# Optimization experiments

Hardware: AMD Instinct MI355X
Metric: run time of the kernel (lower is better)

The kernel has to match this reference:

```python
import jax, jax.numpy as jnp
import numpy as np

B, F, HU, HC = 8192, 100, 128, 512


def _lin(key, din, dout, bias=True, scale=0.02):
    k1, k2 = jax.random.split(key)
    w = jax.random.normal(k1, (din, dout), jnp.float32) * scale
    if bias:
        b = jax.random.normal(k2, (dout,), jnp.float32) * scale
        return w, b
    return (w,)


def setup_inputs() -> dict:
    key = jax.random.key(0)
    ks = jax.random.split(key, 24)
    d = {}
    d['feature_list'] = jax.random.normal(ks[0], (B, F), jnp.float32)
    d['is_treat'] = jax.random.uniform(ks[1], (B,), jnp.float32)
    d['emb'] = jax.random.normal(ks[2], (F, HU), jnp.float32) * 0.02
    d['t_w'], d['t_b'] = _lin(ks[3], 1, HU)
    d['qw'], d['qb'] = _lin(ks[4], HU, HU)
    d['kw'], d['kb'] = _lin(ks[5], HU, HU)
    d['vw'], d['vb'] = _lin(ks[6], HU, HU)
    (d['a1w'],) = _lin(ks[7], HU, HU, bias=False)
    d['a2w'], d['a2b'] = _lin(ks[8], HU, HU)
    (d['a3w'],) = _lin(ks[9], HU, 1, bias=False)
    d['c1w'], d['c1b'] = _lin(ks[10], F * HU, HC)
    d['c2w'], d['c2b'] = _lin(ks[11], HC, HC)
    d['c3w'], d['c3b'] = _lin(ks[12], HC, HC // 2)
    d['c4w'], d['c4b'] = _lin(ks[13], HC // 2, HC // 4)
    d['c5w'], d['c5b'] = _lin(ks[14], HC // 4, HC // 8)
    d['clw'], d['clb'] = _lin(ks[15], HC // 8, 1)
    d['ctw'], d['ctb'] = _lin(ks[16], HC // 8, 1)
    d['u1w'], d['u1b'] = _lin(ks[17], HU, HU)
    d['u2w'], d['u2b'] = _lin(ks[18], HU, HU // 2)
    d['u3w'], d['u3b'] = _lin(ks[19], HU // 2, HU // 4)
    d['u4w'], d['u4b'] = _lin(ks[20], HU // 4, HU // 8)
    d['tlw'], d['tlb'] = _lin(ks[21], HU // 8, 1)
    d['utw'], d['utb'] = _lin(ks[22], HU // 8, 1)
    return d


def reference(feature_list, is_treat, emb, t_w, t_b, qw, qb, kw, kb, vw, vb,
              a1w, a2w, a2b, a3w, c1w, c1b, c2w, c2b, c3w, c3b, c4w, c4b,
              c5w, c5b, clw, clb, ctw, ctb, u1w, u1b, u2w, u2b, u3w, u3b,
              u4w, u4b, tlw, tlb, utw, utb):
    elu = jax.nn.elu
    sig = jax.nn.sigmoid
    b, f = feature_list.shape
    h = emb.shape[1]
    # per-feature embedding: [B, F, H]
    x_rep = feature_list[:, :, None] * emb[None, :, :]
    # normalize over the feature axis (dim=1), as in torch.linalg.norm(dim=1)
    nx = x_rep / jnp.linalg.norm(x_rep, axis=1, keepdims=True)
    # self-attention with sigmoid-then-softmax scores
    Q = nx @ qw + qb
    K = nx @ kw + kb
    V = nx @ vw + vb
    scores = jnp.einsum('bfh,bgh->bfg', Q, K) / (h ** 0.5)
    attn_w = jax.nn.softmax(sig(scores), axis=-1)
    xx = jnp.einsum('bfg,bgh->bfh', attn_w, V).reshape(b, f * h)
    # control net tower
    c = elu(xx @ c1w + c1b)
    c = elu(c @ c2w + c2b)
    c = elu(c @ c3w + c3b)
    c = elu(c @ c4w + c4b)
    c = elu(c @ c5w + c5b)  # is_self=True
    c_logit = c @ clw + clb
    c_tau = c @ ctw + ctb
    c_prob = sig(c_logit)
    # treatment representation: Linear(1, hu) on ones -> [B, H]
    t_rep = jnp.ones((b, 1), feature_list.dtype) @ t_w.reshape(1, h) + t_b
    # interaction attention (vectorized over features)
    att = jax.nn.relu(sig(t_rep @ a1w)[:, None, :] + sig(x_rep @ a2w + a2b))
    att = (att @ a3w)[..., 0]  # [B, F]
    attn = jax.nn.softmax(att, axis=1)
    xt = jnp.einsum('bf,bfh->bh', attn, x_rep)
    # uplift net tower
    u = elu(xt @ u1w + u1b)
    u = elu(u @ u2w + u2b)
    u = elu(u @ u3w + u3b)
    u = elu(u @ u4w + u4b)  # is_self=True
    t_logit = u @ tlw + tlb
    u_tau = u @ utw + utb
    t_prob = sig(t_logit)
    return (c_logit, c_prob, c_tau, t_logit, t_prob, u_tau)
```

## Files before the change

### kernel.cpp

```cpp
#include <hip/hip_runtime.h>
#include <hip/hip_bf16.h>

typedef __bf16 bf16;
typedef __bf16 bf16x8 __attribute__((ext_vector_type(8)));
typedef __bf16 bf16x4 __attribute__((ext_vector_type(4)));
typedef float f32x4 __attribute__((ext_vector_type(4)));
typedef unsigned u32x4 __attribute__((ext_vector_type(4)));

#define DEVI static __device__ __forceinline__

DEVI float sigmoidf_(float x){ return 1.0f/(1.0f+__expf(-x)); }
DEVI float eluf_(float x){ return x>0.f ? x : (__expf(x)-1.f); }
DEVI f32x4 mfma16(bf16x8 a, bf16x8 b, f32x4 c){ return __builtin_amdgcn_mfma_f32_16x16x32_bf16(a,b,c,0,0,0); }
DEVI f32x4 mfma8(long a, long b, f32x4 c){ return __builtin_amdgcn_mfma_f32_16x16x32_fp8_fp8(a,b,c,0,0,0); }
DEVI unsigned pack2_(float a, float b){
    union { bf16 v[2]; unsigned u; } t; t.v[0]=(bf16)a; t.v[1]=(bf16)b; return t.u;
}
DEVI unsigned long long pack4_(float a, float b, float c, float d){
    union { bf16 v[4]; unsigned long long u; } t;
    t.v[0]=(bf16)a; t.v[1]=(bf16)b; t.v[2]=(bf16)c; t.v[3]=(bf16)d; return t.u;
}
DEVI unsigned cvtfp8x4_(float a, float b, float c, float d){
    int v = __builtin_amdgcn_cvt_pk_fp8_f32(a, b, 0, false);
    v = __builtin_amdgcn_cvt_pk_fp8_f32(c, d, v, true);
    return (unsigned)v;
}

#define B_ 8192
#define F_ 100
#define FP 112
#define H_ 128
#define KC_ 12800
#define SPLIT_ 2
#define FP8SC 16.0f

#define SWZ(r,bc) ((bc) ^ (((r)&7)<<4))

DEVI void dotrans_(float (*t)[33], const float* in, bf16* out, int R, int C, int bx, int by, int tid){
    int c0 = bx*32, r0 = by*32;
    int tc = tid & 31, tr = tid >> 5;
    #pragma unroll
    for (int i=0;i<4;i++){
        int r = tr + i*8;
        t[r][tc] = in[(size_t)(r0+r)*C + c0 + tc];
    }
    __syncthreads();
    #pragma unroll
    for (int i=0;i<4;i++){
        int ro = tr + i*8;
        out[(size_t)(c0+ro)*R + r0 + tc] = (bf16)t[tc][ro];
    }
}

__global__ void k_prep_all(const float* __restrict__ qw, const float* __restrict__ qb,
                           const float* __restrict__ kw, const float* __restrict__ kb,
                           const float* __restrict__ tw, const float* __restrict__ tb,
                           const float* __restrict__ a1w, const float* __restrict__ vw,
                           const float* __restrict__ a2w, const float* __restrict__ c2w,
                           const float* __restrict__ c3w,
                           bf16* __restrict__ mextT, float* __restrict__ sigt, float* __restrict__ cconst,
                           bf16* __restrict__ wvT, bf16* __restrict__ wa2t,
                           bf16* __restrict__ c2wt, bf16* __restrict__ c3wt){
    __shared__ float t[32][33];
    const float rsc = 0.08838834764831845f;
    int blk = blockIdx.x, tid = threadIdx.x;
    if (blk < 9){
        #pragma unroll 1
        for (int e=0; e<8; ++e){
            int idx = e*256 + tid;
            int n = blk*16 + (idx>>7), h = idx&127;
            float acc = 0.f;
            if (n < 128){
                for (int d=0; d<128; ++d) acc += qw[h*128+d]*kw[n*128+d];
            } else if (n == 128){
                for (int d=0; d<128; ++d) acc += qw[h*128+d]*kb[d];
            } else if (n == 129){
                for (int d=0; d<128; ++d) acc += kw[h*128+d]*qb[d];
            }
            mextT[n*128+h] = (bf16)(acc*rsc);
        }
    } else if (blk == 9){
        if (tid < 128){
            float acc = 0.f;
            for (int h=0; h<128; ++h) acc += (tw[h]+tb[h]) * a1w[h*128+tid];
            sigt[tid] = sigmoidf_(acc);
        } else if (tid == 128){
            float acc = 0.f;
            for (int d=0; d<128; ++d) acc += qb[d]*kb[d];
            cconst[0] = acc*rsc;
        }
    } else if (blk < 26){
        int i = blk-10; dotrans_(t, vw, wvT, 128,128, i&3, i>>2, tid);
    } else if (blk < 42){
        int i = blk-26; dotrans_(t, a2w, wa2t, 128,128, i&3, i>>2, tid);
    } else if (blk < 298){
        int i = blk-42; dotrans_(t, c2w, c2wt, 512,512, i&15, i>>4, tid);
    } else {
        int i = blk-298; dotrans_(t, c3w, c3wt, 512,256, i&7, i>>3, tid);
    }
}

DEVI int kappa_(int k){
    int f = k>>7, h = k&127;
    if (f < 96)
        return (((f>>4)<<3) | (h>>4))*256 + ((f&15)>>2)*64 + (h&15)*4 + (f&3);
    else
        return 12288 + (h>>4)*64 + (h&15)*4 + (f&3);
}
__global__ void k_tc_kappa8(const float* __restrict__ in, unsigned char* __restrict__ out){
    __shared__ float t[32][33];
    const int C = 512;
    int c0 = blockIdx.x*32, r0 = blockIdx.y*32;
    int tc = threadIdx.x & 31, tr = threadIdx.x >> 5;
    #pragma unroll
    for (int i=0;i<4;i++){
        int r = tr + i*8;
        t[r][tc] = in[(size_t)(r0+r)*C + c0 + tc];
    }
    __syncthreads();
    #pragma unroll
    for (int i=0;i<4;i++){
        int ro = tr + i*8;
        float x = t[tc][ro]*FP8SC;
        int v = __builtin_amdgcn_cvt_pk_fp8_f32(x, x, 0, false);
        out[(size_t)(c0+ro)*KC_ + kappa_(r0+tc)] = (unsigned char)v;
    }
}

__global__ __launch_bounds__(256,2) void k_gatt(
    const float* __restrict__ feat, const float* __restrict__ emb,
    const bf16* __restrict__ wa2t, const float* __restrict__ a2b,
    const float* __restrict__ a3w, const float* __restrict__ sigt,
    float* __restrict__ attg)
{
    __shared__ bf16 sAt[128][136];
    __shared__ bf16 sBt[128][136];
    __shared__ float sRed[2][128];
    int tid=threadIdx.x, w=tid>>6, lane=tid&63, l15=lane&15, l4=lane>>4;
    int m0 = blockIdx.x*128;
    int wr = w>>1, wc = w&1;
    f32x4 acc[4][4];
    #pragma unroll
    for(int mi=0;mi<4;mi++)
        #pragma unroll
        for(int ni=0;ni<4;ni++) acc[mi][ni] = (f32x4){0.f,0.f,0.f,0.f};

    #pragma unroll 2
    for (int t8=0; t8<8; t8++){
        int v = tid + t8*256;
        int row = v>>4, colg = (v&15)*8;
        int gr = m0+row;
        int bb = gr/112, ff = gr - bb*112;
        bf16x8 o;
        if (ff < F_){
            float fv = feat[(size_t)bb*F_ + ff];
            const float* ep = emb + ff*H_ + colg;
            f32x4 e0 = *(const f32x4*)ep;
            f32x4 e1 = *(const f32x4*)(ep+4);
            o[0]=(bf16)(fv*e0[0]); o[1]=(bf16)(fv*e0[1]); o[2]=(bf16)(fv*e0[2]); o[3]=(bf16)(fv*e0[3]);
            o[4]=(bf16)(fv*e1[0]); o[5]=(bf16)(fv*e1[1]); o[6]=(bf16)(fv*e1[2]); o[7]=(bf16)(fv*e1[3]);
        } else {
            #pragma unroll
            for (int e=0;e<8;e++) o[e]=(bf16)0.f;
        }
        *(bf16x8*)&sAt[row][colg] = o;
        *(bf16x8*)&sBt[row][colg] = *(const bf16x8*)(wa2t + row*H_ + colg);
    }
    __syncthreads();
    #pragma unroll
    for(int ks=0;ks<4;ks++){
        bf16x8 af[4], bfr[4];
        #pragma unroll
        for(int mi=0;mi<4;mi++) af[mi] = *(const bf16x8*)&sAt[wr*64+mi*16+l15][ks*32+l4*8];
        #pragma unroll
        for(int ni=0;ni<4;ni++) bfr[ni] = *(const bf16x8*)&sBt[wc*64+ni*16+l15][ks*32+l4*8];
        #pragma unroll
        for(int mi=0;mi<4;mi++)
            #pragma unroll
            for(int ni=0;ni<4;ni++)
                acc[mi][ni] = mfma16(af[mi], bfr[ni], acc[mi][ni]);
    }
    float sg[4], ab[4], a3[4];
    #pragma unroll
    for (int ni=0;ni<4;ni++){
        int n = wc*64 + ni*16 + l15;
        sg[ni]=sigt[n]; ab[ni]=a2b[n]; a3[ni]=a3w[n];
    }
    #pragma unroll
    for (int mi=0;mi<4;mi++){
        float sj[4] = {0.f,0.f,0.f,0.f};
        #pragma unroll
        for (int ni=0;ni<4;ni++){
            #pragma unroll
            for (int j=0;j<4;j++){
                float u = sigmoidf_(acc[mi][ni][j] + ab[ni]);
                float t = sg[ni] + u;
                t = t>0.f ? t : 0.f;
                sj[j] += t*a3[ni];
            }
        }
        #pragma unroll
        for (int j=0;j<4;j++){
            float v = sj[j];
            #pragma unroll
            for (int m=1;m<16;m<<=1) v += __shfl_xor(v,m,16);
            sj[j]=v;
        }
        if (l15==0){
            #pragma unroll
            for (int j=0;j<4;j++) sRed[wc][wr*64+mi*16+l4*4+j] = sj[j];
        }
    }
    __syncthreads();
    if (tid < 128) attg[(size_t)m0 + tid] = sRed[0][tid] + sRed[1][tid];
}

__global__ __launch_bounds__(512,2) void k_attn2(
    const float* __restrict__ feat, const float* __restrict__ emb,
    const bf16* __restrict__ mextT, const bf16* __restrict__ wvT,
    const float* __restrict__ vb, const float* __restrict__ cconst,
    const float* __restrict__ attg,
    unsigned char* __restrict__ xxb, bf16* __restrict__ xtb)
{
    __shared__ char L[81792];
    char* Lm = L;
    char* Ln = L + 32768;
    float* sFeat  = (float*)(L+61440);
    float* sAw    = (float*)(L+61888);
    float* normP  = (float*)(L+62336);
    float* xtP    = (float*)(L+66432);
    float* sNorm  = (float*)(L+79872);
    float* sAlpha = (float*)(L+80384);
    float* sBeta  = (float*)(L+80832);
    float* sInv   = (float*)(L+81280);

    int b = blockIdx.x;
    int tid = threadIdx.x, w = tid>>6, lane = tid&63;
    int l15 = lane&15, l4 = lane>>4;
    bf16 (*sP)[72] = (bf16(*)[72])(L + 61440 + w*2304);

    bf16x8 awv[4];
    #pragma unroll
    for (int kc=0;kc<4;kc++)
        awv[kc] = *(const bf16x8*)(wvT + (w*16+l15)*H_ + kc*32 + l4*8);
    float vbr = vb[w*16+l15];

    #pragma unroll 2
    for (int v = tid; v < 128*16; v += 512){
        int n = v >> 4, cg = (v & 15) * 8;
        *(u32x4*)(Lm + n*256 + SWZ(n, cg*2)) = *(const u32x4*)(mextT + n*128 + cg);
    }
    if (tid < FP) sFeat[tid] = (tid<F_) ? feat[(size_t)b*F_+tid] : 0.f;
    if (w==0){
        const float* ag = attg + (size_t)b*FP;
        float a0 = (lane<F_)? ag[lane] : -1e30f;
        float a1 = (lane+64<F_)? ag[lane+64] : -1e30f;
        float m = fmaxf(a0,a1);
        #pragma unroll
        for(int s=1;s<64;s<<=1) m = fmaxf(m, __shfl_xor(m,s,64));
        float e0 = (lane<F_)? __expf(a0-m):0.f;
        float e1 = (lane+64<F_)? __expf(a1-m):0.f;
        float s = e0+e1;
        #pragma unroll
        for(int t=1;t<64;t<<=1) s += __shfl_xor(s,t,64);
        float inv = 1.f/s;
        if (lane<FP) sAw[lane] = e0*inv;
        if (lane+64<FP) sAw[lane+64] = e1*inv;
    }
    __syncthreads();

    int hp = (tid&63)*2, gg = tid>>6;
    {
        float fa0=0.f, fa1=0.f;
        #pragma unroll 4
        for (int it=0; it<13; ++it){
            int f = gg + 8*it;
            if (f < F_){
                float2 e2 = *(const float2*)(emb + f*H_ + hp);
                float v0 = sFeat[f]*e2.x, v1 = sFeat[f]*e2.y;
                fa0 += v0*v0; fa1 += v1*v1;
            }
        }
        *(float2*)(normP + gg*128 + hp) = make_float2(fa0, fa1);
    }
    __syncthreads();
    if (tid < 128){
        float s = 0.f;
        #pragma unroll
        for (int g2=0; g2<8; ++g2) s += normP[g2*128 + tid];
        sNorm[tid] = sqrtf(s);
    }
    __syncthreads();

    {
        float rn0 = __builtin_amdgcn_rcpf(sNorm[hp]);
        float rn1 = __builtin_amdgcn_rcpf(sNorm[hp+1]);
        #pragma unroll 4
        for (int it=0; it<13; ++it){
            int f = gg + 8*it;
            if (f < F_){
                float2 e2 = *(const float2*)(emb + f*H_ + hp);
                *(unsigned*)(Ln + f*256 + SWZ(f, hp*2)) = pack2_(sFeat[f]*e2.x*rn0, sFeat[f]*e2.y*rn1);
            }
        }
        for (int z=tid; z<768; z+=512){
            int f = 100 + (z>>6), hz = (z&63)*2;
            *(unsigned*)(Ln + f*256 + SWZ(f, hz*2)) = 0u;
        }
    }
    __syncthreads();

    int mt = w;

    if (mt < 7){
        bf16x8 bfr8[4];
        #pragma unroll
        for (int kc=0;kc<4;kc++)
            bfr8[kc] = *(const bf16x8*)(mextT + (128+(l15&1))*H_ + kc*32 + l4*8);
        f32x4 acc = {0.f,0.f,0.f,0.f};
        #pragma unroll
        for (int kc=0;kc<4;kc++){
            bf16x8 a = *(const bf16x8*)(Ln + (mt*16+l15)*256 + SWZ(mt*16+l15, (kc*32+l4*8)*2));
            acc = mfma16(a, bfr8[kc], acc);
        }
        if (l15==0){
            #pragma unroll
            for (int j=0;j<4;j++) sAlpha[mt*16+l4*4+j] = acc[j];
        }
        if (l15==1){
            #pragma unroll
            for (int j=0;j<4;j++) sBeta[mt*16+l4*4+j] = acc[j];
        }
    }
    {
        int g4 = tid>>7, h = tid&127;
        float acc=0.f;
        #pragma unroll 5
        for (int it=0; it<25; ++it){
            int f = g4 + 4*it;
            acc += sAw[f] * (float)*(const bf16*)(Ln + f*256 + SWZ(f, h*2));
        }
        xtP[g4*128+h] = acc;
    }
    __syncthreads();
    if (tid < 128)
        xtb[(size_t)b*H_+tid] = (bf16)((xtP[tid]+xtP[128+tid]+xtP[256+tid]+xtP[384+tid]) * sNorm[tid]);
    __syncthreads();

    const float cc = cconst[0];
    unsigned long long uexB[3];
    if (mt < 7){
        bf16x8 afxi[4];
        #pragma unroll
        for (int kc=0;kc<4;kc++)
            afxi[kc] = *(const bf16x8*)(Ln + (mt*16+l15)*256 + SWZ(mt*16+l15, (kc*32+l4*8)*2));
        f32x4 sc[7];
        #pragma unroll
        for (int gt=0; gt<7; gt++) sc[gt] = (f32x4){0.f,0.f,0.f,0.f};
        #pragma unroll 1
        for (int p=0; p<2; p++){
            #pragma unroll 2
            for (int nt4=0; nt4<4; nt4++){
                int nt = p*4 + nt4;
                bf16x8 bw[4];
                #pragma unroll
                for (int kc=0;kc<4;kc++)
                    bw[kc] = *(const bf16x8*)(Lm + (nt*16+l15)*256 + SWZ(nt*16+l15, (kc*32+l4*8)*2));
                f32x4 d = {0.f,0.f,0.f,0.f};
                #pragma unroll
                for (int kc=0;kc<4;kc++) d = mfma16(bw[kc], afxi[kc], d);
                *(unsigned long long*)(&sP[l15][nt4*16 + l4*4]) = pack4_(d[0],d[1],d[2],d[3]);
            }
            bf16x8 afs0 = *(const bf16x8*)&sP[l15][l4*8];
            bf16x8 afs1 = *(const bf16x8*)&sP[l15][32+l4*8];
            #pragma unroll
            for (int gt=0; gt<7; gt++){
                int r = gt*16+l15;
                bf16x8 b0 = *(const bf16x8*)(Ln + r*256 + SWZ(r, (p*64 + l4*8)*2));
                bf16x8 b1 = *(const bf16x8*)(Ln + r*256 + SWZ(r, (p*64 + 32 + l4*8)*2));
                sc[gt] = mfma16(b0, afs0, sc[gt]);
                sc[gt] = mfma16(b1, afs1, sc[gt]);
            }
        }
        float aj = sAlpha[mt*16+l15];
        float rs = 0.f;
        #pragma unroll
        for (int gt=0; gt<7; gt++){
            f32x4 bt4 = *(const f32x4*)&sBeta[gt*16+l4*4];
            float e[4];
            #pragma unroll
            for (int j=0;j<4;j++){
                int g = gt*16 + l4*4 + j;
                float val = sc[gt][j] + aj + bt4[j] + cc;
                e[j] = (g<F_) ? __expf(sigmoidf_(val)) : 0.f;
                rs += e[j];
            }
            if (gt < 4)
                *(unsigned long long*)(&sP[l15][gt*16 + l4*4]) = pack4_(e[0],e[1],e[2],e[3]);
            else
                uexB[gt-4] = pack4_(e[0],e[1],e[2],e[3]);
        }
        rs += __shfl_xor(rs, 16, 64);
        rs += __shfl_xor(rs, 32, 64);
        if (l4 == 0) sInv[w*16 + l15] = 1.f/rs;
    }

    unsigned long long vpku[7];
    #pragma unroll
    for (int gt=0; gt<7; gt++){
        f32x4 acc = {0.f,0.f,0.f,0.f};
        #pragma unroll
        for (int kc=0;kc<4;kc++){
            int r = gt*16+l15;
            bf16x8 a = *(const bf16x8*)(Ln + r*256 + SWZ(r, (kc*32+l4*8)*2));
            acc = mfma16(a, awv[kc], acc);
        }
        vpku[gt] = pack4_(acc[0]+vbr, acc[1]+vbr, acc[2]+vbr, acc[3]+vbr);
    }
    __syncthreads();

    {
        int hrow = w*16 + l15;
        #pragma unroll
        for (int gt=0; gt<7; gt++)
            *(unsigned long long*)(Lm + hrow*256 + SWZ(hrow, gt*32 + l4*8)) = vpku[gt];
    }
    __syncthreads();

    if (mt < 7){
        bf16x8 ap0 = *(const bf16x8*)&sP[l15][l4*8];
        bf16x8 ap1 = *(const bf16x8*)&sP[l15][32+l4*8];
        f32x4 acc8[8];
        #pragma unroll
        for (int ht=0;ht<8;ht++) acc8[ht] = (f32x4){0.f,0.f,0.f,0.f};
        #pragma unroll
        for (int ht=0; ht<8; ht++){
            int r = ht*16+l15;
            bf16x8 bv0 = *(const bf16x8*)(Lm + r*256 + SWZ(r, (l4*8)*2));
            bf16x8 bv1 = *(const bf16x8*)(Lm + r*256 + SWZ(r, (32+l4*8)*2));
            acc8[ht] = mfma16(ap0, bv0, acc8[ht]);
            acc8[ht] = mfma16(ap1, bv1, acc8[ht]);
        }
        #pragma unroll
        for (int gt=4; gt<7; gt++)
            *(unsigned long long*)(&sP[l15][(gt-4)*16 + l4*4]) = uexB[gt-4];
        *(unsigned long long*)(&sP[l15][48 + l4*4]) = 0ull;
        bf16x8 ap2 = *(const bf16x8*)&sP[l15][l4*8];
        bf16x8 ap3 = *(const bf16x8*)&sP[l15][32+l4*8];
        #pragma unroll
        for (int ht=0; ht<8; ht++){
            int r = ht*16+l15;
            int c2 = 64+l4*8;
            int c3 = 96+l4*8;  if (c3 >= 112) c3 = 96;
            bf16x8 bv2 = *(const bf16x8*)(Lm + r*256 + SWZ(r, c2*2));
            bf16x8 bv3 = *(const bf16x8*)(Lm + r*256 + SWZ(r, c3*2));
            acc8[ht] = mfma16(ap2, bv2, acc8[ht]);
            acc8[ht] = mfma16(ap3, bv3, acc8[ht]);
        }
        float fs[4];
        #pragma unroll
        for (int j=0;j<4;j++) fs[j] = sInv[w*16 + l4*4 + j] * FP8SC;
        #pragma unroll
        for (int ht=0; ht<8; ht++){
            unsigned u = cvtfp8x4_(acc8[ht][0]*fs[0], acc8[ht][1]*fs[1], acc8[ht][2]*fs[2], acc8[ht][3]*fs[3]);
            if (mt < 6){
                *(unsigned*)(xxb + (size_t)b*KC_ + (mt*8+ht)*256 + lane*4) = u;
            } else if (l4 == 0){
                *(unsigned*)(xxb + (size_t)b*KC_ + 12288 + ht*64 + l15*4) = u;
            }
        }
    }
}

__global__ __launch_bounds__(256,2) void k_gemm_fp8(const unsigned char* __restrict__ A,
        const unsigned char* __restrict__ Bt, float* __restrict__ part, int M, int N, int K, int KS)
{
    __shared__ unsigned char sA[128][72];
    __shared__ unsigned char sB[128][72];
    int tid=threadIdx.x, w=tid>>6, lane=tid&63, l15=lane&15, l4=lane>>4;
    int m0 = blockIdx.y*128, n0 = blockIdx.x*128;
    int kbeg = blockIdx.z*KS, kend = kbeg + KS;
    int wr = w>>1, wc = w&1;
    f32x4 acc[4][4];
    #pragma unroll
    for(int mi=0;mi<4;mi++)
        #pragma unroll
        for(int ni=0;ni<4;ni++) acc[mi][ni] = (f32x4){0.f,0.f,0.f,0.f};

    for (int k0=kbeg; k0<kend; k0+=64){
        __syncthreads();
        #pragma unroll
        for (int t2=0;t2<2;t2++){
            int t = tid + t2*256;
            int row=t>>2, col=(t&3)*16;
            *(u32x4*)&sA[row][col] = *(const u32x4*)(A + (size_t)(m0+row)*K + k0 + col);
            *(u32x4*)&sB[row][col] = *(const u32x4*)(Bt + (size_t)(n0+row)*K + k0 + col);
        }
        __syncthreads();
        #pragma unroll
        for(int ks=0;ks<2;ks++){
            long af[4], bfr[4];
            #pragma unroll
            for(int mi=0;mi<4;mi++) af[mi] = *(const long*)&sA[wr*64+mi*16+l15][ks*32+l4*8];
            #pragma unroll
            for(int ni=0;ni<4;ni++) bfr[ni] = *(const long*)&sB[wc*64+ni*16+l15][ks*32+l4*8];
            #pragma unroll
            for(int mi=0;mi<4;mi++)
                #pragma unroll
                for(int ni=0;ni<4;ni++)
                    acc[mi][ni] = mfma8(af[mi], bfr[ni], acc[mi][ni]);
        }
    }
    float* pz = part + (size_t)blockIdx.z*M*N;
    #pragma unroll
    for(int mi=0;mi<4;mi++)
        #pragma unroll
        for(int ni=0;ni<4;ni++){
            int col = n0 + wc*64 + ni*16 + l15;
            #pragma unroll
            for(int j=0;j<4;j++){
                int row = m0 + wr*64 + mi*16 + l4*4 + j;
                pz[(size_t)row*N + col] = acc[mi][ni][j];
            }
        }
}

__global__ void k_c1fin(const float* __restrict__ part, const float* __restrict__ bias,
                        bf16* __restrict__ out){
    const size_t MN = (size_t)B_*512;
    size_t e0 = ((size_t)blockIdx.x*256 + threadIdx.x)*4;
    f32x4 s = *(const f32x4*)(part + e0);
    s += *(const f32x4*)(part + MN + e0);
    f32x4 bb = *(const f32x4*)(bias + (e0 & 511));
    const float ds = 1.0f/(FP8SC*FP8SC);
    unsigned long long u = pack4_(eluf_(s[0]*ds+bb[0]), eluf_(s[1]*ds+bb[1]),
                                  eluf_(s[2]*ds+bb[2]), eluf_(s[3]*ds+bb[3]));
    *(unsigned long long*)(out + e0) = u;
}

template<int BN, bool ELU>
__global__ __launch_bounds__(256,2) void k_gemm(const bf16* __restrict__ A, const bf16* __restrict__ Bt,
        const float* __restrict__ bias, bf16* __restrict__ out, int M, int N, int K)
{
    __shared__ bf16 sAt[128][72];
    __shared__ bf16 sBt[BN][72];
    int tid=threadIdx.x, w=tid>>6, lane=tid&63, l15=lane&15, l4=lane>>4;
    int m0 = blockIdx.y*128, n0 = blockIdx.x*BN;
    constexpr int MI = (BN==128)?4:2;
    constexpr int NI = (BN==128)?4:BN/16;
    int wr = (BN==128)? (w>>1) : w;
    int wc = (BN==128)? (w&1) : 0;
    f32x4 acc[MI][NI];
    #pragma unroll
    for(int mi=0;mi<MI;mi++)
        #pragma unroll
        for(int ni=0;ni<NI;ni++) acc[mi][ni] = (f32x4){0.f,0.f,0.f,0.f};

    for (int k0=0; k0<K; k0+=64){
        __syncthreads();
        for (int t=tid; t<128*8; t+=256){
            int row=t>>3, col=(t&7)*8;
            *(bf16x8*)&sAt[row][col] = *(const bf16x8*)(A + (size_t)(m0+row)*K + k0 + col);
        }
        for (int t=tid; t<BN*8; t+=256){
            int row=t>>3, col=(t&7)*8;
            *(bf16x8*)&sBt[row][col] = *(const bf16x8*)(Bt + (size_t)(n0+row)*K + k0 + col);
        }
        __syncthreads();
        #pragma unroll
        for(int ks=0;ks<2;ks++){
            bf16x8 af[MI], bfr[NI];
            #pragma unroll
            for(int mi=0;mi<MI;mi++) af[mi] = *(const bf16x8*)&sAt[wr*(MI*16)+mi*16+l15][ks*32+l4*8];
            #pragma unroll
            for(int ni=0;ni<NI;ni++) bfr[ni] = *(const bf16x8*)&sBt[wc*64+ni*16+l15][ks*32+l4*8];
            #pragma unroll
            for(int mi=0;mi<MI;mi++)
                #pragma unroll
                for(int ni=0;ni<NI;ni++)
                    acc[mi][ni] = mfma16(af[mi], bfr[ni], acc[mi][ni]);
        }
    }
    #pragma unroll
    for(int mi=0;mi<MI;mi++)
        #pragma unroll
        for(int ni=0;ni<NI;ni++){
            int col = n0 + wc*64 + ni*16 + l15;
            float bc = bias[col];
            #pragma unroll
            for(int j=0;j<4;j++){
                int row = m0 + wr*(MI*16) + mi*16 + l4*4 + j;
                float v = acc[mi][ni][j] + bc;
                if (ELU) v = eluf_(v);
                out[(size_t)row*N + col] = (bf16)v;
            }
        }
}

__global__ __launch_bounds__(256,2) void k_ctail(const bf16* __restrict__ c3o,
    const float* __restrict__ c4w, const float* __restrict__ c4b,
    const float* __restrict__ c5w, const float* __restrict__ c5b,
    const float* __restrict__ clw, const float* __restrict__ clb,
    const float* __restrict__ ctw, const float* __restrict__ ctb, float* __restrict__ outp)
{
    __shared__ float sA[32][260];
    __shared__ float sB[32][132];
    __shared__ float sC[32][68];
    int tid = threadIdx.x; int r0 = blockIdx.x*32;
    for (int v=tid; v<32*64; v+=256){
        int r=v>>6, c=(v&63)*4;
        bf16x4 x = *(const bf16x4*)(c3o + (size_t)(r0+r)*256 + c);
        sA[r][c]=(float)x[0]; sA[r][c+1]=(float)x[1]; sA[r][c+2]=(float)x[2]; sA[r][c+3]=(float)x[3];
    }
    __syncthreads();
    {
        int j = tid&127, rb = tid>>7;
        float acc[16];
        #pragma unroll
        for (int i=0;i<16;i++) acc[i]=c4b[j];
        #pragma unroll 4
        for (int h=0;h<256;h++){
            float wv = c4w[h*128+j];
            #pragma unroll
            for (int i=0;i<16;i++) acc[i] += sA[2*i+rb][h]*wv;
        }
        #pragma unroll
        for (int i=0;i<16;i++) sB[2*i+rb][j] = eluf_(acc[i]);
    }
    __syncthreads();
    {
        int j = tid&63, rb = tid>>6;
        float acc[8];
        #pragma unroll
        for (int i=0;i<8;i++) acc[i]=c5b[j];
        #pragma unroll 4
        for (int h=0;h<128;h++){
            float wv = c5w[h*64+j];
            #pragma unroll
            for (int i=0;i<8;i++) acc[i] += sB[4*i+rb][h]*wv;
        }
        #pragma unroll
        for (int i=0;i<8;i++) sC[4*i+rb][j] = eluf_(acc[i]);
    }
    __syncthreads();
    if (tid < 32){
        float r1 = clb[0], r2 = ctb[0];
        #pragma unroll 8
        for (int k=0;k<64;k++){ float v = sC[tid][k]; r1 += v*clw[k]; r2 += v*ctw[k]; }
        int row = r0 + tid;
        outp[row] = r1;
        outp[B_ + row] = sigmoidf_(r1);
        outp[(size_t)2*B_ + row] = r2;
    }
}

__global__ __launch_bounds__(256,2) void k_utower(const bf16* __restrict__ xtb,
    const float* __restrict__ u1w, const float* __restrict__ u1b,
    const float* __restrict__ u2w, const float* __restrict__ u2b,
    const float* __restrict__ u3w, const float* __restrict__ u3b,
    const float* __restrict__ u4w, const float* __restrict__ u4b,
    const float* __restrict__ tlw, const float* __restrict__ tlb,
    const float* __restrict__ utw, const float* __restrict__ utb, float* __restrict__ outp)
{
    __shared__ float sA[32][132];
    __shared__ float sB[32][132];
    __shared__ float sC[32][68];
    __shared__ float sD[32][36];
    __shared__ float sE[32][20];
    int tid = threadIdx.x; int r0 = blockIdx.x*32;
    for (int v=tid; v<32*32; v+=256){
        int r=v>>5, c=(v&31)*4;
        bf16x4 x = *(const bf16x4*)(xtb + (size_t)(r0+r)*128 + c);
        sA[r][c]=(float)x[0]; sA[r][c+1]=(float)x[1]; sA[r][c+2]=(float)x[2]; sA[r][c+3]=(float)x[3];
    }
    __syncthreads();
    {
        int j = tid&127, rb = tid>>7;
        float acc[16];
        #pragma unroll
        for (int i=0;i<16;i++) acc[i]=u1b[j];
        #pragma unroll 4
        for (int h=0;h<128;h++){
            float wv = u1w[h*128+j];
            #pragma unroll
            for (int i=0;i<16;i++) acc[i] += sA[2*i+rb][h]*wv;
        }
        #pragma unroll
        for (int i=0;i<16;i++) sB[2*i+rb][j] = eluf_(acc[i]);
    }
    __syncthreads();
    {
        int j = tid&63, rb = tid>>6;
        float acc[8];
        #pragma unroll
        for (int i=0;i<8;i++) acc[i]=u2b[j];
        #pragma unroll 4
        for (int h=0;h<128;h++){
            float wv = u2w[h*64+j];
            #pragma unroll
            for (int i=0;i<8;i++) acc[i] += sB[4*i+rb][h]*wv;
        }
        #pragma unroll
        for (int i=0;i<8;i++) sC[4*i+rb][j] = eluf_(acc[i]);
    }
    __syncthreads();
    {
        int j = tid&31, rb = tid>>5;
        float acc[4];
        #pragma unroll
        for (int i=0;i<4;i++) acc[i]=u3b[j];
        #pragma unroll 4
        for (int h=0;h<64;h++){
            float wv = u3w[h*32+j];
            #pragma unroll
            for (int i=0;i<4;i++) acc[i] += sC[8*i+rb][h]*wv;
        }
        #pragma unroll
        for (int i=0;i<4;i++) sD[8*i+rb][j] = eluf_(acc[i]);
    }
    __syncthreads();
    {
        int j = tid&15, rb = tid>>4;
        float acc0=u4b[j], acc1=u4b[j];
        #pragma unroll 4
        for (int h=0;h<32;h++){
            float wv = u4w[h*16+j];
            acc0 += sD[rb][h]*wv;
            acc1 += sD[16+rb][h]*wv;
        }
        sE[rb][j] = eluf_(acc0);
        sE[16+rb][j] = eluf_(acc1);
    }
    __syncthreads();
    if (tid < 32){
        float r1 = tlb[0], r2 = utb[0];
        #pragma unroll
        for (int k=0;k<16;k++){ float v = sE[tid][k]; r1 += v*tlw[k]; r2 += v*utw[k]; }
        int row = r0 + tid;
        outp[(size_t)3*B_ + row] = r1;
        outp[(size_t)4*B_ + row] = sigmoidf_(r1);
        outp[(size_t)5*B_ + row] = r2;
    }
}

extern "C" void kernel_launch(void* const* d_in, const int* in_sizes, int n_in,
                              void* d_out, int out_size, void* d_ws, size_t ws_size,
                              hipStream_t stream) {
    const float* feat=(const float*)d_in[0];
    const float* emb =(const float*)d_in[2];
    const float* t_w =(const float*)d_in[3]; const float* t_b=(const float*)d_in[4];
    const float* qw  =(const float*)d_in[5]; const float* qb =(const float*)d_in[6];
    const float* kw  =(const float*)d_in[7]; const float* kb =(const float*)d_in[8];
    const float* vw  =(const float*)d_in[9]; const float* vb =(const float*)d_in[10];
    const float* a1w =(const float*)d_in[11];
    const float* a2w =(const float*)d_in[12]; const float* a2b=(const float*)d_in[13];
    const float* a3w =(const float*)d_in[14];
    const float* c1w =(const float*)d_in[15]; const float* c1b=(const float*)d_in[16];
    const float* c2w =(const float*)d_in[17]; const float* c2b=(const float*)d_in[18];
    const float* c3w =(const float*)d_in[19]; const float* c3b=(const float*)d_in[20];
    const float* c4w =(const float*)d_in[21]; const float* c4b=(const float*)d_in[22];
    const float* c5w =(const float*)d_in[23]; const float* c5b=(const float*)d_in[24];
    const float* clw =(const float*)d_in[25]; const float* clb=(const float*)d_in[26];
    const float* ctw =(const float*)d_in[27]; const float* ctb=(const float*)d_in[28];
    const float* u1w =(const float*)d_in[29]; const float* u1b=(const float*)d_in[30];
    const float* u2w =(const float*)d_in[31]; const float* u2b=(const float*)d_in[32];
    const float* u3w =(const float*)d_in[33]; const float* u3b=(const float*)d_in[34];
    const float* u4w =(const float*)d_in[35]; const float* u4b=(const float*)d_in[36];
    const float* tlw =(const float*)d_in[37]; const float* tlb=(const float*)d_in[38];
    const float* utw =(const float*)d_in[39]; const float* utb=(const float*)d_in[40];
    float* outp = (float*)d_out;

    char* ws = (char*)d_ws;
    size_t off = 0;
    auto alloc = [&](size_t bytes)->char*{ char* p = ws + off; off += (bytes + 255) & ~(size_t)255; return p; };
    unsigned char* xxb = (unsigned char*)alloc((size_t)B_*KC_);
    float* part  = (float*)alloc((size_t)SPLIT_*B_*512*4);
    float* attg  = (float*)alloc((size_t)B_*FP*4);
    bf16* xtb    = (bf16*)alloc((size_t)B_*128*2);
    bf16* cbuf1  = (bf16*)alloc((size_t)B_*512*2);
    bf16* mextT  = (bf16*)alloc(144*128*2);
    bf16* wvT    = (bf16*)alloc(128*128*2);
    bf16* wa2t   = (bf16*)alloc(128*128*2);
    unsigned char* c1wtk8 = (unsigned char*)alloc((size_t)512*KC_);
    bf16* c2wt   = (bf16*)alloc((size_t)512*512*2);
    bf16* c3wt   = (bf16*)alloc((size_t)512*256*2);
    float* sigt  = (float*)alloc(128*4);
    float* cconst= (float*)alloc(4);
    bf16* cbuf2 = (bf16*)(xxb);
    bf16* cbuf3 = (bf16*)(xxb + (16u<<20));
    (void)ws_size; (void)in_sizes; (void)n_in; (void)out_size;

    k_prep_all<<<426,256,0,stream>>>(qw,qb,kw,kb,t_w,t_b,a1w, vw, a2w, c2w, c3w,
                                     mextT, sigt, cconst, wvT, wa2t, c2wt, c3wt);
    k_tc_kappa8<<<dim3(16,400),256,0,stream>>>(c1w, c1wtk8);

    k_gatt<<<7168,256,0,stream>>>(feat, emb, wa2t, a2b, a3w, sigt, attg);

    k_attn2<<<B_,512,0,stream>>>(feat,emb,mextT,wvT,vb,cconst,attg, xxb, xtb);

    k_utower<<<256,256,0,stream>>>(xtb,u1w,u1b,u2w,u2b,u3w,u3b,u4w,u4b,tlw,tlb,utw,utb,outp);

    k_gemm_fp8<<<dim3(4,64,SPLIT_),256,0,stream>>>(xxb, c1wtk8, part, B_,512,KC_, KC_/SPLIT_);
    k_c1fin<<<4096,256,0,stream>>>(part, c1b, cbuf1);

    k_gemm<128,true><<<dim3(4,64),256,0,stream>>>(cbuf1, c2wt, c2b, cbuf2, B_,512,512);
    k_gemm<128,true><<<dim3(2,64),256,0,stream>>>(cbuf2, c3wt, c3b, cbuf3, B_,256,512);
    k_ctail<<<256,256,0,stream>>>(cbuf3,c4w,c4b,c5w,c5b,clw,clb,ctw,ctb,outp);
}
```

Baseline: 729.3 us.

## Merge weight transpose with gating kernel, fuse tower tails, raise split-K

```diff
diff --git a/kernel.cpp b/kernel.cpp
--- a/kernel.cpp
+++ b/kernel.cpp
@@ -31,7 +31,7 @@
 #define FP 112
 #define H_ 128
 #define KC_ 12800
-#define SPLIT_ 2
+#define SPLIT_ 4
 #define FP8SC 16.0f
 
 #define SWZ(r,bc) ((bc) ^ (((r)&7)<<4))
@@ -107,37 +107,41 @@
     else
         return 12288 + (h>>4)*64 + (h&15)*4 + (f&3);
 }
-__global__ void k_tc_kappa8(const float* __restrict__ in, unsigned char* __restrict__ out){
-    __shared__ float t[32][33];
-    const int C = 512;
-    int c0 = blockIdx.x*32, r0 = blockIdx.y*32;
-    int tc = threadIdx.x & 31, tr = threadIdx.x >> 5;
-    #pragma unroll
-    for (int i=0;i<4;i++){
-        int r = tr + i*8;
-        t[r][tc] = in[(size_t)(r0+r)*C + c0 + tc];
-    }
-    __syncthreads();
-    #pragma unroll
-    for (int i=0;i<4;i++){
-        int ro = tr + i*8;
-        float x = t[tc][ro]*FP8SC;
-        int v = __builtin_amdgcn_cvt_pk_fp8_f32(x, x, 0, false);
-        out[(size_t)(c0+ro)*KC_ + kappa_(r0+tc)] = (unsigned char)v;
-    }
-}
-
-__global__ __launch_bounds__(256,2) void k_gatt(
+
+__global__ __launch_bounds__(256,2) void k_gk(
+    const float* __restrict__ c1w, unsigned char* __restrict__ c1wtk8,
     const float* __restrict__ feat, const float* __restrict__ emb,
     const bf16* __restrict__ wa2t, const float* __restrict__ a2b,
     const float* __restrict__ a3w, const float* __restrict__ sigt,
     float* __restrict__ attg)
 {
-    __shared__ bf16 sAt[128][136];
-    __shared__ bf16 sBt[128][136];
-    __shared__ float sRed[2][128];
-    int tid=threadIdx.x, w=tid>>6, lane=tid&63, l15=lane&15, l4=lane>>4;
-    int m0 = blockIdx.x*128;
+    __shared__ char A[37888];
+    int blk = blockIdx.x, tid = threadIdx.x;
+    if (blk < 6400){
+        float (*t)[33] = (float(*)[33])A;
+        const int C = 512;
+        int c0 = (blk&15)*32, r0 = (blk>>4)*32;
+        int tc = tid & 31, tr = tid >> 5;
+        #pragma unroll
+        for (int i=0;i<4;i++){
+            int r = tr + i*8;
+            t[r][tc] = c1w[(size_t)(r0+r)*C + c0 + tc];
+        }
+        __syncthreads();
+        #pragma unroll
+        for (int i=0;i<4;i++){
+            int ro = tr + i*8;
+            float x = t[tc][ro]*FP8SC;
+            int v = __builtin_amdgcn_cvt_pk_fp8_f32(x, x, 0, false);
+            c1wtk8[(size_t)(c0+ro)*KC_ + kappa_(r0+tc)] = (unsigned char)v;
+        }
+        return;
+    }
+    bf16 (*sAt)[72] = (bf16(*)[72])A;
+    bf16 (*sBt)[72] = (bf16(*)[72])(A + 18432);
+    float (*sRed)[128] = (float(*)[128])(A + 36864);
+    int w=tid>>6, lane=tid&63, l15=lane&15, l4=lane>>4;
+    int m0 = (blk-6400)*128;
     int wr = w>>1, wc = w&1;
     f32x4 acc[4][4];
     #pragma unroll
@@ -145,40 +149,44 @@
         #pragma unroll
         for(int ni=0;ni<4;ni++) acc[mi][ni] = (f32x4){0.f,0.f,0.f,0.f};
 
-    #pragma unroll 2
-    for (int t8=0; t8<8; t8++){
-        int v = tid + t8*256;
-        int row = v>>4, colg = (v&15)*8;
-        int gr = m0+row;
-        int bb = gr/112, ff = gr - bb*112;
-        bf16x8 o;
-        if (ff < F_){
-            float fv = feat[(size_t)bb*F_ + ff];
-            const float* ep = emb + ff*H_ + colg;
-            f32x4 e0 = *(const f32x4*)ep;
-            f32x4 e1 = *(const f32x4*)(ep+4);
-            o[0]=(bf16)(fv*e0[0]); o[1]=(bf16)(fv*e0[1]); o[2]=(bf16)(fv*e0[2]); o[3]=(bf16)(fv*e0[3]);
-            o[4]=(bf16)(fv*e1[0]); o[5]=(bf16)(fv*e1[1]); o[6]=(bf16)(fv*e1[2]); o[7]=(bf16)(fv*e1[3]);
-        } else {
-            #pragma unroll
-            for (int e=0;e<8;e++) o[e]=(bf16)0.f;
-        }
-        *(bf16x8*)&sAt[row][colg] = o;
-        *(bf16x8*)&sBt[row][colg] = *(const bf16x8*)(wa2t + row*H_ + colg);
-    }
-    __syncthreads();
-    #pragma unroll
-    for(int ks=0;ks<4;ks++){
-        bf16x8 af[4], bfr[4];
-        #pragma unroll
-        for(int mi=0;mi<4;mi++) af[mi] = *(const bf16x8*)&sAt[wr*64+mi*16+l15][ks*32+l4*8];
-        #pragma unroll
-        for(int ni=0;ni<4;ni++) bfr[ni] = *(const bf16x8*)&sBt[wc*64+ni*16+l15][ks*32+l4*8];
-        #pragma unroll
-        for(int mi=0;mi<4;mi++)
-            #pragma unroll
-            for(int ni=0;ni<4;ni++)
-                acc[mi][ni] = mfma16(af[mi], bfr[ni], acc[mi][ni]);
+    #pragma unroll 1
+    for (int k0=0; k0<128; k0+=64){
+        __syncthreads();
+        #pragma unroll
+        for (int t4=0; t4<4; t4++){
+            int t = tid + t4*256;
+            int row=t>>3, col=(t&7)*8;
+            int gr = m0+row;
+            int bb = gr/112, ff = gr - bb*112;
+            bf16x8 o;
+            if (ff < F_){
+                float fv = feat[(size_t)bb*F_ + ff];
+                const float* ep = emb + ff*H_ + k0 + col;
+                f32x4 e0 = *(const f32x4*)ep;
+                f32x4 e1 = *(const f32x4*)(ep+4);
+                o[0]=(bf16)(fv*e0[0]); o[1]=(bf16)(fv*e0[1]); o[2]=(bf16)(fv*e0[2]); o[3]=(bf16)(fv*e0[3]);
+                o[4]=(bf16)(fv*e1[0]); o[5]=(bf16)(fv*e1[1]); o[6]=(bf16)(fv*e1[2]); o[7]=(bf16)(fv*e1[3]);
+            } else {
+                #pragma unroll
+                for (int e=0;e<8;e++) o[e]=(bf16)0.f;
+            }
+            *(bf16x8*)&sAt[row][col] = o;
+            *(bf16x8*)&sBt[row][col] = *(const bf16x8*)(wa2t + row*H_ + k0 + col);
+        }
+        __syncthreads();
+        #pragma unroll
+        for(int ks=0;ks<2;ks++){
+            bf16x8 af[4], bfr[4];
+            #pragma unroll
+            for(int mi=0;mi<4;mi++) af[mi] = *(const bf16x8*)&sAt[wr*64+mi*16+l15][ks*32+l4*8];
+            #pragma unroll
+            for(int ni=0;ni<4;ni++) bfr[ni] = *(const bf16x8*)&sBt[wc*64+ni*16+l15][ks*32+l4*8];
+            #pragma unroll
+            for(int mi=0;mi<4;mi++)
+                #pragma unroll
+                for(int ni=0;ni<4;ni++)
+                    acc[mi][ni] = mfma16(af[mi], bfr[ni], acc[mi][ni]);
+        }
     }
     float sg[4], ab[4], a3[4];
     #pragma unroll
@@ -226,9 +234,8 @@
     char* Lm = L;
     char* Ln = L + 32768;
     float* sFeat  = (float*)(L+61440);
-    float* sAw    = (float*)(L+61888);
     float* normP  = (float*)(L+62336);
-    float* xtP    = (float*)(L+66432);
+    float* sAw    = (float*)(L+77568);
     float* sNorm  = (float*)(L+79872);
     float* sAlpha = (float*)(L+80384);
     float* sBeta  = (float*)(L+80832);
@@ -332,19 +339,6 @@
             for (int j=0;j<4;j++) sBeta[mt*16+l4*4+j] = acc[j];
         }
     }
-    {
-        int g4 = tid>>7, h = tid&127;
-        float acc=0.f;
-        #pragma unroll 5
-        for (int it=0; it<25; ++it){
-            int f = g4 + 4*it;
-            acc += sAw[f] * (float)*(const bf16*)(Ln + f*256 + SWZ(f, h*2));
-        }
-        xtP[g4*128+h] = acc;
-    }
-    __syncthreads();
-    if (tid < 128)
-        xtb[(size_t)b*H_+tid] = (bf16)((xtP[tid]+xtP[128+tid]+xtP[256+tid]+xtP[384+tid]) * sNorm[tid]);
     __syncthreads();
 
     const float cc = cconst[0];
@@ -403,6 +397,17 @@
         rs += __shfl_xor(rs, 16, 64);
         rs += __shfl_xor(rs, 32, 64);
         if (l4 == 0) sInv[w*16 + l15] = 1.f/rs;
+    } else {
+        int h = lane;
+        float a0=0.f, a1=0.f;
+        #pragma unroll 4
+        for (int f=0; f<F_; ++f){
+            float awf = sAw[f];
+            a0 += awf * (float)*(const bf16*)(Ln + f*256 + SWZ(f, h*2));
+            a1 += awf * (float)*(const bf16*)(Ln + f*256 + SWZ(f, (h+64)*2));
+        }
+        xtb[(size_t)b*H_ + h]      = (bf16)(a0 * sNorm[h]);
+        xtb[(size_t)b*H_ + h + 64] = (bf16)(a1 * sNorm[h+64]);
     }
 
     unsigned long long vpku[7];
@@ -531,6 +536,8 @@
     size_t e0 = ((size_t)blockIdx.x*256 + threadIdx.x)*4;
     f32x4 s = *(const f32x4*)(part + e0);
     s += *(const f32x4*)(part + MN + e0);
+    s += *(const f32x4*)(part + 2*MN + e0);
+    s += *(const f32x4*)(part + 3*MN + e0);
     f32x4 bb = *(const f32x4*)(bias + (e0 & 511));
     const float ds = 1.0f/(FP8SC*FP8SC);
     unsigned long long u = pack4_(eluf_(s[0]*ds+bb[0]), eluf_(s[1]*ds+bb[1]),
@@ -597,64 +604,12 @@
         }
 }
 
-__global__ __launch_bounds__(256,2) void k_ctail(const bf16* __restrict__ c3o,
+__global__ __launch_bounds__(256,2) void k_tails(const bf16* __restrict__ c3o,
     const float* __restrict__ c4w, const float* __restrict__ c4b,
     const float* __restrict__ c5w, const float* __restrict__ c5b,
     const float* __restrict__ clw, const float* __restrict__ clb,
-    const float* __restrict__ ctw, const float* __restrict__ ctb, float* __restrict__ outp)
-{
-    __shared__ float sA[32][260];
-    __shared__ float sB[32][132];
-    __shared__ float sC[32][68];
-    int tid = threadIdx.x; int r0 = blockIdx.x*32;
-    for (int v=tid; v<32*64; v+=256){
-        int r=v>>6, c=(v&63)*4;
-        bf16x4 x = *(const bf16x4*)(c3o + (size_t)(r0+r)*256 + c);
-        sA[r][c]=(float)x[0]; sA[r][c+1]=(float)x[1]; sA[r][c+2]=(float)x[2]; sA[r][c+3]=(float)x[3];
-    }
-    __syncthreads();
-    {
-        int j = tid&127, rb = tid>>7;
-        float acc[16];
-        #pragma unroll
-        for (int i=0;i<16;i++) acc[i]=c4b[j];
-        #pragma unroll 4
-        for (int h=0;h<256;h++){
-            float wv = c4w[h*128+j];
-            #pragma unroll
-            for (int i=0;i<16;i++) acc[i] += sA[2*i+rb][h]*wv;
-        }
-        #pragma unroll
-        for (int i=0;i<16;i++) sB[2*i+rb][j] = eluf_(acc[i]);
-    }
-    __syncthreads();
-    {
-        int j = tid&63, rb = tid>>6;
-        float acc[8];
-        #pragma unroll
-        for (int i=0;i<8;i++) acc[i]=c5b[j];
-        #pragma unroll 4
-        for (int h=0;h<128;h++){
-            float wv = c5w[h*64+j];
-            #pragma unroll
-            for (int i=0;i<8;i++) acc[i] += sB[4*i+rb][h]*wv;
-        }
-        #pragma unroll
-        for (int i=0;i<8;i++) sC[4*i+rb][j] = eluf_(acc[i]);
-    }
-    __syncthreads();
-    if (tid < 32){
-        float r1 = clb[0], r2 = ctb[0];
-        #pragma unroll 8
-        for (int k=0;k<64;k++){ float v = sC[tid][k]; r1 += v*clw[k]; r2 += v*ctw[k]; }
-        int row = r0 + tid;
-        outp[row] = r1;
-        outp[B_ + row] = sigmoidf_(r1);
-        outp[(size_t)2*B_ + row] = r2;
-    }
-}
-
-__global__ __launch_bounds__(256,2) void k_utower(const bf16* __restrict__ xtb,
+    const float* __restrict__ ctw, const float* __restrict__ ctb,
+    const bf16* __restrict__ xtb,
     const float* __restrict__ u1w, const float* __restrict__ u1b,
     const float* __restrict__ u2w, const float* __restrict__ u2b,
     const float* __restrict__ u3w, const float* __restrict__ u3b,
@@ -662,84 +617,137 @@
     const float* __restrict__ tlw, const float* __restrict__ tlb,
     const float* __restrict__ utw, const float* __restrict__ utb, float* __restrict__ outp)
 {
-    __shared__ float sA[32][132];
-    __shared__ float sB[32][132];
-    __shared__ float sC[32][68];
-    __shared__ float sD[32][36];
-    __shared__ float sE[32][20];
-    int tid = threadIdx.x; int r0 = blockIdx.x*32;
-    for (int v=tid; v<32*32; v+=256){
-        int r=v>>5, c=(v&31)*4;
-        bf16x4 x = *(const bf16x4*)(xtb + (size_t)(r0+r)*128 + c);
-        sA[r][c]=(float)x[0]; sA[r][c+1]=(float)x[1]; sA[r][c+2]=(float)x[2]; sA[r][c+3]=(float)x[3];
-    }
-    __syncthreads();
-    {
-        int j = tid&127, rb = tid>>7;
-        float acc[16];
-        #pragma unroll
-        for (int i=0;i<16;i++) acc[i]=u1b[j];
-        #pragma unroll 4
-        for (int h=0;h<128;h++){
-            float wv = u1w[h*128+j];
-            #pragma unroll
-            for (int i=0;i<16;i++) acc[i] += sA[2*i+rb][h]*wv;
-        }
-        #pragma unroll
-        for (int i=0;i<16;i++) sB[2*i+rb][j] = eluf_(acc[i]);
-    }
-    __syncthreads();
-    {
-        int j = tid&63, rb = tid>>6;
-        float acc[8];
-        #pragma unroll
-        for (int i=0;i<8;i++) acc[i]=u2b[j];
-        #pragma unroll 4
-        for (int h=0;h<128;h++){
-            float wv = u2w[h*64+j];
-            #pragma unroll
-            for (int i=0;i<8;i++) acc[i] += sB[4*i+rb][h]*wv;
-        }
-        #pragma unroll
-        for (int i=0;i<8;i++) sC[4*i+rb][j] = eluf_(acc[i]);
-    }
-    __syncthreads();
-    {
-        int j = tid&31, rb = tid>>5;
-        float acc[4];
-        #pragma unroll
-        for (int i=0;i<4;i++) acc[i]=u3b[j];
-        #pragma unroll 4
-        for (int h=0;h<64;h++){
-            float wv = u3w[h*32+j];
-            #pragma unroll
-            for (int i=0;i<4;i++) acc[i] += sC[8*i+rb][h]*wv;
-        }
-        #pragma unroll
-        for (int i=0;i<4;i++) sD[8*i+rb][j] = eluf_(acc[i]);
-    }
-    __syncthreads();
-    {
-        int j = tid&15, rb = tid>>4;
-        float acc0=u4b[j], acc1=u4b[j];
-        #pragma unroll 4
-        for (int h=0;h<32;h++){
-            float wv = u4w[h*16+j];
-            acc0 += sD[rb][h]*wv;
-            acc1 += sD[16+rb][h]*wv;
-        }
-        sE[rb][j] = eluf_(acc0);
-        sE[16+rb][j] = eluf_(acc1);
-    }
-    __syncthreads();
-    if (tid < 32){
-        float r1 = tlb[0], r2 = utb[0];
-        #pragma unroll
-        for (int k=0;k<16;k++){ float v = sE[tid][k]; r1 += v*tlw[k]; r2 += v*utw[k]; }
-        int row = r0 + tid;
-        outp[(size_t)3*B_ + row] = r1;
-        outp[(size_t)4*B_ + row] = sigmoidf_(r1);
-        outp[(size_t)5*B_ + row] = r2;
+    __shared__ char A[58880];
+    int tid = threadIdx.x, blk = blockIdx.x;
+    int r0 = (blk>>1)*32;
+    if ((blk & 1) == 0){
+        float (*sA)[260] = (float(*)[260])A;
+        float (*sB)[132] = (float(*)[132])(A + 33280);
+        float (*sC)[68]  = (float(*)[68])(A + 50176);
+        for (int v=tid; v<32*64; v+=256){
+            int r=v>>6, c=(v&63)*4;
+            bf16x4 x = *(const bf16x4*)(c3o + (size_t)(r0+r)*256 + c);
+            sA[r][c]=(float)x[0]; sA[r][c+1]=(float)x[1]; sA[r][c+2]=(float)x[2]; sA[r][c+3]=(float)x[3];
+        }
+        __syncthreads();
+        {
+            int j = tid&127, rb = tid>>7;
+            float acc[16];
+            #pragma unroll
+            for (int i=0;i<16;i++) acc[i]=c4b[j];
+            #pragma unroll 4
+            for (int h=0;h<256;h++){
+                float wv = c4w[h*128+j];
+                #pragma unroll
+                for (int i=0;i<16;i++) acc[i] += sA[2*i+rb][h]*wv;
+            }
+            #pragma unroll
+            for (int i=0;i<16;i++) sB[2*i+rb][j] = eluf_(acc[i]);
+        }
+        __syncthreads();
+        {
+            int j = tid&63, rb = tid>>6;
+            float acc[8];
+            #pragma unroll
+            for (int i=0;i<8;i++) acc[i]=c5b[j];
+            #pragma unroll 4
+            for (int h=0;h<128;h++){
+                float wv = c5w[h*64+j];
+                #pragma unroll
+                for (int i=0;i<8;i++) acc[i] += sB[4*i+rb][h]*wv;
+            }
+            #pragma unroll
+            for (int i=0;i<8;i++) sC[4*i+rb][j] = eluf_(acc[i]);
+        }
+        __syncthreads();
+        if (tid < 32){
+            float r1 = clb[0], r2 = ctb[0];
+            #pragma unroll 8
+            for (int k=0;k<64;k++){ float v = sC[tid][k]; r1 += v*clw[k]; r2 += v*ctw[k]; }
+            int row = r0 + tid;
+            outp[row] = r1;
+            outp[B_ + row] = sigmoidf_(r1);
+            outp[(size_t)2*B_ + row] = r2;
+        }
+    } else {
+        float (*sA)[132] = (float(*)[132])A;
+        float (*sB)[132] = (float(*)[132])(A + 16896);
+        float (*sC)[68]  = (float(*)[68])(A + 33792);
+        float (*sD)[36]  = (float(*)[36])(A + 42496);
+        float (*sE)[20]  = (float(*)[20])(A + 47104);
+        for (int v=tid; v<32*32; v+=256){
+            int r=v>>5, c=(v&31)*4;
+            bf16x4 x = *(const bf16x4*)(xtb + (size_t)(r0+r)*128 + c);
+            sA[r][c]=(float)x[0]; sA[r][c+1]=(float)x[1]; sA[r][c+2]=(float)x[2]; sA[r][c+3]=(float)x[3];
+        }
+        __syncthreads();
+        {
+            int j = tid&127, rb = tid>>7;
+            float acc[16];
+            #pragma unroll
+            for (int i=0;i<16;i++) acc[i]=u1b[j];
+            #pragma unroll 4
+            for (int h=0;h<128;h++){
+                float wv = u1w[h*128+j];
+                #pragma unroll
+                for (int i=0;i<16;i++) acc[i] += sA[2*i+rb][h]*wv;
+            }
+            #pragma unroll
+            for (int i=0;i<16;i++) sB[2*i+rb][j] = eluf_(acc[i]);
+        }
+        __syncthreads();
+        {
+            int j = tid&63, rb = tid>>6;
+            float acc[8];
+            #pragma unroll
+            for (int i=0;i<8;i++) acc[i]=u2b[j];
+            #pragma unroll 4
+            for (int h=0;h<128;h++){
+                float wv = u2w[h*64+j];
+                #pragma unroll
+                for (int i=0;i<8;i++) acc[i] += sB[4*i+rb][h]*wv;
+            }
+            #pragma unroll
+            for (int i=0;i<8;i++) sC[4*i+rb][j] = eluf_(acc[i]);
+        }
+        __syncthreads();
+        {
+            int j = tid&31, rb = tid>>5;
+            float acc[4];
+            #pragma unroll
+            for (int i=0;i<4;i++) acc[i]=u3b[j];
+            #pragma unroll 4
+            for (int h=0;h<64;h++){
+                float wv = u3w[h*32+j];
+                #pragma unroll
+                for (int i=0;i<4;i++) acc[i] += sC[8*i+rb][h]*wv;
+            }
+            #pragma unroll
+            for (int i=0;i<4;i++) sD[8*i+rb][j] = eluf_(acc[i]);
+        }
+        __syncthreads();
+        {
+            int j = tid&15, rb = tid>>4;
+            float acc0=u4b[j], acc1=u4b[j];
+            #pragma unroll 4
+            for (int h=0;h<32;h++){
+                float wv = u4w[h*16+j];
+                acc0 += sD[rb][h]*wv;
+                acc1 += sD[16+rb][h]*wv;
+            }
+            sE[rb][j] = eluf_(acc0);
+            sE[16+rb][j] = eluf_(acc1);
+        }
+        __syncthreads();
+        if (tid < 32){
+            float r1 = tlb[0], r2 = utb[0];
+            #pragma unroll
+            for (int k=0;k<16;k++){ float v = sE[tid][k]; r1 += v*tlw[k]; r2 += v*utw[k]; }
+            int row = r0 + tid;
+            outp[(size_t)3*B_ + row] = r1;
+            outp[(size_t)4*B_ + row] = sigmoidf_(r1);
+            outp[(size_t)5*B_ + row] = r2;
+        }
     }
 }
 
@@ -792,18 +800,17 @@
 
     k_prep_all<<<426,256,0,stream>>>(qw,qb,kw,kb,t_w,t_b,a1w, vw, a2w, c2w, c3w,
                                      mextT, sigt, cconst, wvT, wa2t, c2wt, c3wt);
-    k_tc_kappa8<<<dim3(16,400),256,0,stream>>>(c1w, c1wtk8);
-
-    k_gatt<<<7168,256,0,stream>>>(feat, emb, wa2t, a2b, a3w, sigt, attg);
+
+    k_gk<<<13568,256,0,stream>>>(c1w, c1wtk8, feat, emb, wa2t, a2b, a3w, sigt, attg);
 
     k_attn2<<<B_,512,0,stream>>>(feat,emb,mextT,wvT,vb,cconst,attg, xxb, xtb);
-
-    k_utower<<<256,256,0,stream>>>(xtb,u1w,u1b,u2w,u2b,u3w,u3b,u4w,u4b,tlw,tlb,utw,utb,outp);
 
     k_gemm_fp8<<<dim3(4,64,SPLIT_),256,0,stream>>>(xxb, c1wtk8, part, B_,512,KC_, KC_/SPLIT_);
     k_c1fin<<<4096,256,0,stream>>>(part, c1b, cbuf1);
 
     k_gemm<128,true><<<dim3(4,64),256,0,stream>>>(cbuf1, c2wt, c2b, cbuf2, B_,512,512);
     k_gemm<128,true><<<dim3(2,64),256,0,stream>>>(cbuf2, c3wt, c3b, cbuf3, B_,256,512);
-    k_ctail<<<256,256,0,stream>>>(cbuf3,c4w,c4b,c5w,c5b,clw,clb,ctw,ctb,outp);
-}
+
+    k_tails<<<512,256,0,stream>>>(cbuf3,c4w,c4b,c5w,c5b,clw,clb,ctw,ctb,
+                                  xtb,u1w,u1b,u2w,u2b,u3w,u3b,u4w,u4b,tlw,tlb,utw,utb,outp);
+}
```

Result: faster. 645.6 us (-11.5%).
